# Kernel tuning notes

Measured on AMD Instinct MI355X. Metric: run time of the kernel, lower is better.

Reference implementation:

```python
import jax, jax.numpy as jnp
import numpy as np

B, C_IN, IMG = 4, 1, 256
E, P = 800, 4            # embed_size, patch_size
H, DH, M = 8, 64, 64     # heads, dim_head=heads**2, num_landmarks
N = (IMG // P) ** 2      # 4096 tokens
OUT = 256                # output_size
RESK = 33                # lucidrains residual depthwise conv kernel
BN_EPS = 1e-5
LN_EPS = 1e-5
PINV_ITERS = 6


def setup_inputs() -> dict:
    key = jax.random.key(0)
    ks = iter(jax.random.split(key, 32))
    def nrm(shape, s=0.02):
        return jax.random.normal(next(ks), shape, jnp.float32) * s
    inp = {"x": jax.random.normal(next(ks), (B, C_IN, IMG, IMG), jnp.float32)}
    # conv stack: (in, out, kernel); last conv has stride=P, padding=0
    for i, (ci, co, kk) in enumerate([(C_IN, 64, 3), (64, 128, 3), (128, 256, 3), (256, E, P)]):
        inp[f"w{i}"] = nrm((co, ci, kk, kk), 0.05)
        inp[f"b{i}"] = jnp.zeros((co,), jnp.float32)
        inp[f"g{i}"] = jnp.ones((co,), jnp.float32)    # BN gamma
        inp[f"be{i}"] = jnp.zeros((co,), jnp.float32)  # BN beta
        inp[f"mu{i}"] = nrm((co,), 0.1)                # BN running mean
        inp[f"var{i}"] = jax.random.uniform(next(ks), (co,), jnp.float32, 0.5, 1.5)
    inp["qkv_w"] = nrm((E, 3 * H * DH))      # to_qkv (no bias)
    inp["out_w"] = nrm((H * DH, E))          # to_out linear
    inp["out_b"] = jnp.zeros((E,), jnp.float32)
    inp["res_w"] = nrm((H, 1, RESK, 1), 0.05)  # depthwise residual conv over token dim
    inp["ln_g"] = jnp.ones((E,), jnp.float32)
    inp["ln_b"] = jnp.zeros((E,), jnp.float32)
    inp["head_w"] = nrm((E, OUT * OUT // N))   # Linear(800, 16)
    inp["head_b"] = jnp.zeros((OUT * OUT // N,), jnp.float32)
    return inp


def conv2d(x, w, b, stride, pad):
    y = jax.lax.conv_general_dilated(x, w, (stride, stride), [(pad, pad), (pad, pad)],
                                     dimension_numbers=("NCHW", "OIHW", "NCHW"))
    return y + b[None, :, None, None]


def bn(x, g, be, mu, var):
    s = g * jax.lax.rsqrt(var + BN_EPS)  # eval-mode BatchNorm
    return x * s[None, :, None, None] + (be - mu * s)[None, :, None, None]


def moore_penrose_pinv(a, iters=PINV_ITERS):
    I = jnp.eye(a.shape[-1], dtype=a.dtype)
    z = jnp.swapaxes(a, -1, -2) / (jnp.max(jnp.abs(a).sum(-1)) * jnp.max(jnp.abs(a).sum(-2)))
    for _ in range(iters):
        az = a @ z
        z = 0.25 * z @ (13.0 * I - az @ (15.0 * I - az @ (7.0 * I - az)))
    return z


def reference(x, w0, b0, g0, be0, mu0, var0, w1, b1, g1, be1, mu1, var1,
              w2, b2, g2, be2, mu2, var2, w3, b3, g3, be3, mu3, var3,
              qkv_w, out_w, out_b, res_w, ln_g, ln_b, head_w, head_b):
    # ---- PatchEmbedConv ----
    h = x
    blocks = [(w0, b0, g0, be0, mu0, var0, 1, 1), (w1, b1, g1, be1, mu1, var1, 1, 1),
              (w2, b2, g2, be2, mu2, var2, 1, 1), (w3, b3, g3, be3, mu3, var3, P, 0)]
    for w, b, g, be, mu, var, st, pd in blocks:
        h = jax.nn.relu(bn(conv2d(h, w, b, st, pd), g, be, mu, var))
    tok = h.reshape(B, E, N).transpose(0, 2, 1)  # [B, N, E]

    # ---- NystromAttention (n % m == 0, so no front padding needed) ----
    qkv = tok @ qkv_w  # [B, N, 3*H*DH]
    q, k, v = [t.reshape(B, N, H, DH).transpose(0, 2, 1, 3) for t in jnp.split(qkv, 3, axis=-1)]
    q = q * (DH ** -0.5)
    l = N // M
    q_l = q.reshape(B, H, M, l, DH).mean(3)  # landmark means over consecutive blocks
    k_l = k.reshape(B, H, M, l, DH).mean(3)
    a1 = jax.nn.softmax(jnp.einsum("bhnd,bhmd->bhnm", q, k_l), axis=-1)    # [B,H,N,M]
    a2 = jax.nn.softmax(jnp.einsum("bhmd,bhkd->bhmk", q_l, k_l), axis=-1)  # [B,H,M,M]
    a3 = jax.nn.softmax(jnp.einsum("bhmd,bhnd->bhmn", q_l, k), axis=-1)    # [B,H,M,N]
    out = (a1 @ moore_penrose_pinv(a2)) @ (a3 @ v)  # [B,H,N,DH]
    # residual depthwise conv over the token dim of v (groups = heads)
    res = jax.lax.conv_general_dilated(v, res_w, (1, 1), [(RESK // 2, RESK // 2), (0, 0)],
                                       dimension_numbers=("NCHW", "OIHW", "NCHW"),
                                       feature_group_count=H)
    out = out + res
    out = out.transpose(0, 2, 1, 3).reshape(B, N, H * DH)
    out = out @ out_w + out_b  # [B, N, E]

    # ---- LayerNorm ----
    mu_t = out.mean(-1, keepdims=True)
    var_t = out.var(-1, keepdims=True)
    out = (out - mu_t) * jax.lax.rsqrt(var_t + LN_EPS) * ln_g + ln_b

    # ---- reconstruction head ----
    y = jax.nn.sigmoid(out @ head_w + head_b)  # [B, N, OUT*OUT/N]
    return y.reshape(-1, 1, OUT, OUT)
```

## Files before the change

### kernel.cpp

```cpp
#include <hip/hip_runtime.h>

#define DI __device__ __forceinline__

constexpr float BN_EPS_C = 1e-5f;
constexpr float LN_EPS_C = 1e-5f;

typedef _Float16 half8 __attribute__((ext_vector_type(8)));
typedef float f32x4 __attribute__((ext_vector_type(4)));

constexpr size_t B_H0   = 0;
constexpr size_t B_H1   = 8388608;
constexpr size_t B_H2   = 25165824;
constexpr size_t B_Q    = 25165824;
constexpr size_t B_V    = 58720256;
constexpr size_t B_KT   = 75497472;
constexpr size_t B_ATT  = 92274688;
constexpr size_t B_LNB  = 25165824;
constexpr size_t B_TOK  = 159383552;
constexpr size_t B_WP1  = 185597952;
constexpr size_t B_WP2  = 185745408;
constexpr size_t B_WP3  = 186335232;
constexpr size_t B_QKVT = 192888832;
constexpr size_t B_OWT  = 195346432;
constexpr size_t B_QL   = 196165632;
constexpr size_t B_KL   = 196689920;
constexpr size_t B_KLH  = 197214208;
constexpr size_t B_A2   = 197476352;
constexpr size_t B_W2T  = 198524928;
constexpr size_t B_A3V  = 198787072;
constexpr size_t B_SCAL = 199311360;
constexpr size_t B_HWH  = 199311424;

DI float blockReduceSum(float v) {
  #pragma unroll
  for (int o = 32; o; o >>= 1) v += __shfl_xor(v, o);
  __shared__ float red[4];
  int w = threadIdx.x >> 6;
  __syncthreads();
  if ((threadIdx.x & 63) == 0) red[w] = v;
  __syncthreads();
  return red[0] + red[1] + red[2] + red[3];
}

template <int LP, int RP>
DI void mm16v(const float* L, const float* R, int r0, int c0, float reg[4][4]) {
  #pragma unroll
  for (int i = 0; i < 4; ++i)
    #pragma unroll
    for (int j = 0; j < 4; ++j) reg[i][j] = 0.f;
  #pragma unroll 4
  for (int dd = 0; dd < 64; dd += 4) {
    f32x4 l[4], rv[4];
    #pragma unroll
    for (int i = 0; i < 4; ++i)
      l[i] = *reinterpret_cast<const f32x4*>(&L[(size_t)(r0 + i) * LP + dd]);
    #pragma unroll
    for (int u = 0; u < 4; ++u)
      rv[u] = *reinterpret_cast<const f32x4*>(&R[(size_t)(dd + u) * RP + c0]);
    #pragma unroll
    for (int i = 0; i < 4; ++i)
      #pragma unroll
      for (int u = 0; u < 4; ++u)
        #pragma unroll
        for (int j = 0; j < 4; ++j)
          reg[i][j] = fmaf(l[i][u], rv[u][j], reg[i][j]);
  }
}

__global__ void k_pack_all(
    const float* __restrict__ w1, const float* __restrict__ w2c, const float* __restrict__ w3,
    const float* __restrict__ qkvw, const float* __restrict__ outw, const float* __restrict__ headw,
    _Float16* __restrict__ wp1, _Float16* __restrict__ wp2, _Float16* __restrict__ wp3,
    _Float16* __restrict__ qkvT, _Float16* __restrict__ owT, _Float16* __restrict__ hwh,
    float* __restrict__ scal) {
  size_t i = (size_t)blockIdx.x * 256 + threadIdx.x;
  if (i < 73728) {
    int q = i % 9, ci = (i / 9) % 64, co = i / (9 * 64);
    wp1[((size_t)co * 9 + q) * 64 + ci] = (_Float16)w1[i];
  } else if (i < 368640) {
    size_t j = i - 73728;
    int q = j % 9, ci = (j / 9) % 128, co = j / (9 * 128);
    wp2[((size_t)co * 9 + q) * 128 + ci] = (_Float16)w2c[j];
  } else if (i < 3645440) {
    size_t j = i - 368640;
    int q = j % 16, ci = (j / 16) % 256, co = j / (16 * 256);
    wp3[((size_t)co * 16 + q) * 256 + ci] = (_Float16)w3[j];
  } else if (i < 4874240) {
    size_t j = i - 3645440;
    int n = j % 1536, k = j / 1536;
    qkvT[(size_t)n * 800 + k] = (_Float16)qkvw[j];
  } else if (i < 5283840) {
    size_t j = i - 4874240;
    int n = j % 800, k = j / 800;
    owT[(size_t)n * 512 + k] = (_Float16)outw[j];
  } else if (i < 5296640) {
    size_t j = i - 5283840;
    int n = j % 16, k = j / 16;
    hwh[(size_t)n * 800 + k] = (_Float16)headw[j];
  } else if (i < 5296642) {
    scal[i - 5296640] = 0.f;
  }
}

__global__ __launch_bounds__(256) void k_conv0(
    const float* __restrict__ xb, const float* __restrict__ w0, const float* __restrict__ b0,
    const float* __restrict__ g0, const float* __restrict__ be0, const float* __restrict__ mu0,
    const float* __restrict__ var0, _Float16* __restrict__ h0) {
  const int t = threadIdx.x, co = t & 63, xg = t >> 6;
  const int y = blockIdx.x;
  const int x0 = blockIdx.y * 64 + xg * 16;
  float wreg[9];
  #pragma unroll
  for (int q = 0; q < 9; ++q) wreg[q] = w0[co * 9 + q];
  float s = g0[co] * rsqrtf(var0[co] + BN_EPS_C);
  float sh = fmaf(b0[co] - mu0[co], s, be0[co]);
  #pragma unroll 4
  for (int xl = 0; xl < 16; ++xl) {
    int xx = x0 + xl;
    float acc = 0.f;
    #pragma unroll
    for (int dy = 0; dy < 3; ++dy) {
      int yy = y + dy - 1;
      if ((unsigned)yy >= 256u) continue;
      #pragma unroll
      for (int dx = 0; dx < 3; ++dx) {
        int xi = xx + dx - 1;
        if ((unsigned)xi >= 256u) continue;
        acc = fmaf(wreg[dy * 3 + dx], xb[yy * 256 + xi], acc);
      }
    }
    float v = fmaxf(fmaf(acc, s, sh), 0.f);
    h0[((size_t)y * 256 + xx) * 64 + co] = (_Float16)v;
  }
}

template <int CI>
__global__ __launch_bounds__(256) void k_convs(
    const _Float16* __restrict__ in, const _Float16* __restrict__ wp,
    const float* __restrict__ bias, const float* __restrict__ g, const float* __restrict__ be,
    const float* __restrict__ mu, const float* __restrict__ var,
    _Float16* __restrict__ out, int CO, int NCT) {
  __shared__ _Float16 Ab[2][128 * 40];
  __shared__ _Float16 Bb[2][128 * 40];
  constexpr int CPQ = CI / 32;
  constexpr int NCK = 9 * CPQ;
  const int t = threadIdx.x;
  const int bid = blockIdx.x;
  const int xcd = bid & 7, slot = bid >> 3;
  const int pj = slot / NCT, cc = slot % NCT;
  const int p = pj * 8 + xcd;
  const int r0 = p * 128, c0 = cc * 128;

  const int ma = t >> 2, kga = t & 3;
  int ry[2], rx[2];
  #pragma unroll
  for (int s = 0; s < 2; ++s) {
    int r = r0 + ma + s * 64;
    ry[s] = r >> 8;
    rx[s] = r & 255;
  }
  const _Float16* baseB[2];
  #pragma unroll
  for (int s = 0; s < 2; ++s)
    baseB[s] = wp + (size_t)(c0 + ma + s * 64) * 9 * CI + kga * 8;
  const int wo = ma * 40 + kga * 8;

  auto loadA = [&](int s, int ck) -> half8 {
    int q = ck / CPQ, coff = (ck % CPQ) * 32;
    int yy = ry[s] + q / 3 - 1;
    int xx = rx[s] + q % 3 - 1;
    half8 a = {};
    if ((unsigned)yy < 256u && (unsigned)xx < 256u)
      a = *reinterpret_cast<const half8*>(in + ((size_t)yy * 256 + xx) * CI + coff + kga * 8);
    return a;
  };

  {
    half8 a0 = loadA(0, 0), a1 = loadA(1, 0);
    half8 b0v = *reinterpret_cast<const half8*>(baseB[0]);
    half8 b1v = *reinterpret_cast<const half8*>(baseB[1]);
    *reinterpret_cast<half8*>(&Ab[0][wo]) = a0;
    *reinterpret_cast<half8*>(&Ab[0][wo + 2560]) = a1;
    *reinterpret_cast<half8*>(&Bb[0][wo]) = b0v;
    *reinterpret_cast<half8*>(&Bb[0][wo + 2560]) = b1v;
  }
  __syncthreads();

  const int w = t >> 6, lo = t & 15, hi = (t >> 4) & 3;
  const int wm = w >> 1, wn = w & 1;
  const int roA = (wm * 64 + lo) * 40 + 8 * hi;
  const int roB = (wn * 64 + lo) * 40 + 8 * hi;
  f32x4 acc[4][4] = {};

  for (int ck = 0; ck < NCK; ++ck) {
    const int cur = ck & 1;
    const bool more = (ck + 1 < NCK);
    half8 rA0, rA1, rB0, rB1;
    if (more) {
      rA0 = loadA(0, ck + 1);
      rA1 = loadA(1, ck + 1);
      rB0 = *reinterpret_cast<const half8*>(baseB[0] + (ck + 1) * 32);
      rB1 = *reinterpret_cast<const half8*>(baseB[1] + (ck + 1) * 32);
    }
    half8 af[4], bf[4];
    #pragma unroll
    for (int mi = 0; mi < 4; ++mi)
      af[mi] = *reinterpret_cast<const half8*>(&Ab[cur][roA + mi * 640]);
    #pragma unroll
    for (int ni = 0; ni < 4; ++ni)
      bf[ni] = *reinterpret_cast<const half8*>(&Bb[cur][roB + ni * 640]);
    #pragma unroll
    for (int mi = 0; mi < 4; ++mi)
      #pragma unroll
      for (int ni = 0; ni < 4; ++ni)
        acc[mi][ni] = __builtin_amdgcn_mfma_f32_16x16x32_f16(af[mi], bf[ni], acc[mi][ni], 0, 0, 0);
    if (more) {
      *reinterpret_cast<half8*>(&Ab[cur ^ 1][wo]) = rA0;
      *reinterpret_cast<half8*>(&Ab[cur ^ 1][wo + 2560]) = rA1;
      *reinterpret_cast<half8*>(&Bb[cur ^ 1][wo]) = rB0;
      *reinterpret_cast<half8*>(&Bb[cur ^ 1][wo + 2560]) = rB1;
    }
    __syncthreads();
  }

  #pragma unroll
  for (int ni = 0; ni < 4; ++ni) {
    int co = c0 + wn * 64 + ni * 16 + lo;
    float s = g[co] * rsqrtf(var[co] + BN_EPS_C);
    float sh = fmaf(bias[co] - mu[co], s, be[co]);
    #pragma unroll
    for (int mi = 0; mi < 4; ++mi)
      #pragma unroll
      for (int rr = 0; rr < 4; ++rr) {
        int row = r0 + wm * 64 + mi * 16 + hi * 4 + rr;
        float v = fmaxf(fmaf(acc[mi][ni][rr], s, sh), 0.f);
        out[(size_t)row * CO + co] = (_Float16)v;
      }
  }
}

__global__ __launch_bounds__(256) void k_c3(
    const _Float16* __restrict__ h2, const _Float16* __restrict__ wp3,
    const float* __restrict__ b3, const float* __restrict__ g3, const float* __restrict__ be3,
    const float* __restrict__ mu3, const float* __restrict__ var3,
    _Float16* __restrict__ tok) {
  __shared__ _Float16 Abuf[2][128 * 40];
  __shared__ _Float16 Bbuf[2][160 * 40];
  const int t = threadIdx.x;
  const int bid = blockIdx.x;
  const int xcd = bid & 7, slot = bid >> 3;
  const int pj = slot / 5, cc = slot % 5;
  const int p = pj * 8 + xcd;
  const int r0 = p * 128, c0 = cc * 160;
  const int img = r0 >> 12;
  const _Float16* h2i = h2 + (size_t)img * 16777216;

  const int ma = t >> 2, kga = t & 3;
  const _Float16* baseA[2];
  #pragma unroll
  for (int s = 0; s < 2; ++s) {
    int m = ma + s * 64;
    int r = r0 + m;
    int py = (r & 4095) >> 6, px = r & 63;
    baseA[s] = h2i + ((size_t)py * 1024 + px * 4) * 256 + kga * 8;
  }
  const _Float16* baseB[3];
  #pragma unroll
  for (int s = 0; s < 3; ++s) {
    int cb = ma + s * 64;
    baseB[s] = wp3 + (size_t)(c0 + (cb < 160 ? cb : 159)) * 4096 + kga * 8;
  }
  const int wo = ma * 40 + kga * 8;

  const int w = t >> 6, lo = t & 15, hi = (t >> 4) & 3;
  const int wm = w >> 1, wn = w & 1;
  const int roA = (wm * 64 + lo) * 40 + 8 * hi;
  const int roB = (wn * 80 + lo) * 40 + 8 * hi;

  f32x4 acc[4][5] = {};

  {
    half8 a0 = *reinterpret_cast<const half8*>(baseA[0]);
    half8 a1 = *reinterpret_cast<const half8*>(baseA[1]);
    half8 b0v = *reinterpret_cast<const half8*>(baseB[0]);
    half8 b1v = *reinterpret_cast<const half8*>(baseB[1]);
    *reinterpret_cast<half8*>(&Abuf[0][wo]) = a0;
    *reinterpret_cast<half8*>(&Abuf[0][wo + 2560]) = a1;
    *reinterpret_cast<half8*>(&Bbuf[0][wo]) = b0v;
    *reinterpret_cast<half8*>(&Bbuf[0][wo + 2560]) = b1v;
    if (t < 128) {
      half8 b2v = *reinterpret_cast<const half8*>(baseB[2]);
      *reinterpret_cast<half8*>(&Bbuf[0][wo + 5120]) = b2v;
    }
  }
  __syncthreads();

  for (int ck = 0; ck < 128; ++ck) {
    const int cur = ck & 1;
    const bool more = (ck + 1 < 128);
    half8 rA0, rA1, rB0, rB1, rB2;
    if (more) {
      const int kn = (ck + 1) << 5;
      const int q = kn >> 8, qk = kn & 255;
      const int aoff = (q >> 2) * 65536 + (q & 3) * 256 + qk;
      rA0 = *reinterpret_cast<const half8*>(baseA[0] + aoff);
      rA1 = *reinterpret_cast<const half8*>(baseA[1] + aoff);
      rB0 = *reinterpret_cast<const half8*>(baseB[0] + kn);
      rB1 = *reinterpret_cast<const half8*>(baseB[1] + kn);
      if (t < 128) rB2 = *reinterpret_cast<const half8*>(baseB[2] + kn);
    }
    half8 af[4], bf[5];
    #pragma unroll
    for (int mi = 0; mi < 4; ++mi)
      af[mi] = *reinterpret_cast<const half8*>(&Abuf[cur][roA + mi * 640]);
    #pragma unroll
    for (int ni = 0; ni < 5; ++ni)
      bf[ni] = *reinterpret_cast<const half8*>(&Bbuf[cur][roB + ni * 640]);
    #pragma unroll
    for (int mi = 0; mi < 4; ++mi)
      #pragma unroll
      for (int ni = 0; ni < 5; ++ni)
        acc[mi][ni] = __builtin_amdgcn_mfma_f32_16x16x32_f16(af[mi], bf[ni], acc[mi][ni], 0, 0, 0);
    if (more) {
      *reinterpret_cast<half8*>(&Abuf[cur ^ 1][wo]) = rA0;
      *reinterpret_cast<half8*>(&Abuf[cur ^ 1][wo + 2560]) = rA1;
      *reinterpret_cast<half8*>(&Bbuf[cur ^ 1][wo]) = rB0;
      *reinterpret_cast<half8*>(&Bbuf[cur ^ 1][wo + 2560]) = rB1;
      if (t < 128) *reinterpret_cast<half8*>(&Bbuf[cur ^ 1][wo + 5120]) = rB2;
    }
    __syncthreads();
  }

  #pragma unroll
  for (int ni = 0; ni < 5; ++ni) {
    int col = c0 + wn * 80 + ni * 16 + lo;
    float s = g3[col] * rsqrtf(var3[col] + BN_EPS_C);
    float sh = fmaf(b3[col] - mu3[col], s, be3[col]);
    #pragma unroll
    for (int mi = 0; mi < 4; ++mi)
      #pragma unroll
      for (int rr = 0; rr < 4; ++rr) {
        int row = r0 + wm * 64 + mi * 16 + hi * 4 + rr;
        float v = fmaxf(fmaf(acc[mi][ni][rr], s, sh), 0.f);
        tok[(size_t)row * 800 + col] = (_Float16)v;
      }
  }
}

__global__ __launch_bounds__(256) void k_qkv_s(
    const _Float16* __restrict__ tok, const _Float16* __restrict__ qkvT,
    _Float16* __restrict__ qx, _Float16* __restrict__ kTg, _Float16* __restrict__ vx,
    float* __restrict__ ql, float* __restrict__ kl, _Float16* __restrict__ klh) {
  __shared__ _Float16 SH[20480];
  _Float16* AbP = SH;
  _Float16* BbP = SH + 10240;
  const int t = threadIdx.x;
  const int bid = blockIdx.x;
  const int xcd = bid & 7, slot = bid >> 3;
  const int pj = slot / 12, cc = slot % 12;
  const int p = pj * 8 + xcd;
  const int r0 = p * 128, c0 = cc * 128;

  const int ma = t >> 2, kga = t & 3;
  const _Float16* baseA[2];
  const _Float16* baseB[2];
  #pragma unroll
  for (int s = 0; s < 2; ++s) {
    baseA[s] = tok + (size_t)(r0 + ma + s * 64) * 800 + kga * 8;
    baseB[s] = qkvT + (size_t)(c0 + ma + s * 64) * 800 + kga * 8;
  }
  const int wo = ma * 40 + kga * 8;

  {
    half8 a0 = *reinterpret_cast<const half8*>(baseA[0]);
    half8 a1 = *reinterpret_cast<const half8*>(baseA[1]);
    half8 b0v = *reinterpret_cast<const half8*>(baseB[0]);
    half8 b1v = *reinterpret_cast<const half8*>(baseB[1]);
    *reinterpret_cast<half8*>(&AbP[wo]) = a0;
    *reinterpret_cast<half8*>(&AbP[wo + 2560]) = a1;
    *reinterpret_cast<half8*>(&BbP[wo]) = b0v;
    *reinterpret_cast<half8*>(&BbP[wo + 2560]) = b1v;
  }
  __syncthreads();

  const int w = t >> 6, lo = t & 15, hi = (t >> 4) & 3;
  const int wm = w >> 1, wn = w & 1;
  const int roA = (wm * 64 + lo) * 40 + 8 * hi;
  const int roB = (wn * 64 + lo) * 40 + 8 * hi;
  f32x4 acc[4][4] = {};

  for (int ck = 0; ck < 25; ++ck) {
    const int cur = ck & 1;
    const bool more = (ck + 1 < 25);
    half8 rA0, rA1, rB0, rB1;
    if (more) {
      const int kn = (ck + 1) * 32;
      rA0 = *reinterpret_cast<const half8*>(baseA[0] + kn);
      rA1 = *reinterpret_cast<const half8*>(baseA[1] + kn);
      rB0 = *reinterpret_cast<const half8*>(baseB[0] + kn);
      rB1 = *reinterpret_cast<const half8*>(baseB[1] + kn);
    }
    half8 af[4], bf[4];
    #pragma unroll
    for (int mi = 0; mi < 4; ++mi)
      af[mi] = *reinterpret_cast<const half8*>(&AbP[cur * 5120 + roA + mi * 640]);
    #pragma unroll
    for (int ni = 0; ni < 4; ++ni)
      bf[ni] = *reinterpret_cast<const half8*>(&BbP[cur * 5120 + roB + ni * 640]);
    #pragma unroll
    for (int mi = 0; mi < 4; ++mi)
      #pragma unroll
      for (int ni = 0; ni < 4; ++ni)
        acc[mi][ni] = __builtin_amdgcn_mfma_f32_16x16x32_f16(af[mi], bf[ni], acc[mi][ni], 0, 0, 0);
    if (more) {
      *reinterpret_cast<half8*>(&AbP[(cur ^ 1) * 5120 + wo]) = rA0;
      *reinterpret_cast<half8*>(&AbP[(cur ^ 1) * 5120 + wo + 2560]) = rA1;
      *reinterpret_cast<half8*>(&BbP[(cur ^ 1) * 5120 + wo]) = rB0;
      *reinterpret_cast<half8*>(&BbP[(cur ^ 1) * 5120 + wo + 2560]) = rB1;
    }
    __syncthreads();
  }

  const int seg = cc >> 2;
  const int b = r0 >> 12;
  const int m = ((r0 & 4095) >> 6) + wm;
  if (seg == 1) {
    #pragma unroll
    for (int ni = 0; ni < 4; ++ni) {
      int cl = wn * 64 + ni * 16 + lo;
      #pragma unroll
      for (int mi = 0; mi < 4; ++mi)
        #pragma unroll
        for (int rr = 0; rr < 4; ++rr) {
          int nl = wm * 64 + mi * 16 + hi * 4 + rr;
          SH[cl * 136 + nl] = (_Float16)acc[mi][ni][rr];
        }
    }
    __syncthreads();
    const int base_row = b * 512 + (cc & 3) * 128;
    const int base_n = (p & 31) * 128;
    #pragma unroll
    for (int e = t; e < 2048; e += 256) {
      int cl = e >> 4, ch = e & 15;
      half8 vvv = *reinterpret_cast<const half8*>(&SH[cl * 136 + ch * 8]);
      *reinterpret_cast<half8*>(&kTg[(size_t)(base_row + cl) * 4096 + base_n + ch * 8]) = vvv;
    }
  } else {
    const float scale = (seg == 0) ? 0.125f : 1.0f;
    _Float16* dst = (seg == 0) ? qx : vx;
    #pragma unroll
    for (int ni = 0; ni < 4; ++ni) {
      int cseg = (cc & 3) * 128 + wn * 64 + ni * 16 + lo;
      int h = cseg >> 6, d = cseg & 63;
      #pragma unroll
      for (int mi = 0; mi < 4; ++mi)
        #pragma unroll
        for (int rr = 0; rr < 4; ++rr) {
          int row = r0 + wm * 64 + mi * 16 + hi * 4 + rr;
          int nn = row & 4095;
          dst[((size_t)(b * 8 + h) * 4096 + nn) * 64 + d] = (_Float16)(acc[mi][ni][rr] * scale);
        }
    }
  }
  if (seg <= 1) {
    const float lscale = ((seg == 0) ? 0.125f : 1.0f) * (1.f / 64.f);
    #pragma unroll
    for (int ni = 0; ni < 4; ++ni) {
      float sum = 0.f;
      #pragma unroll
      for (int mi = 0; mi < 4; ++mi)
        #pragma unroll
        for (int rr = 0; rr < 4; ++rr) sum += acc[mi][ni][rr];
      sum += __shfl_xor(sum, 16);
      sum += __shfl_xor(sum, 32);
      if (hi == 0) {
        int cseg = (cc & 3) * 128 + wn * 64 + ni * 16 + lo;
        int h = cseg >> 6, d = cseg & 63;
        int bh = b * 8 + h;
        float lm = sum * lscale;
        if (seg == 0) {
          ql[((size_t)bh * 64 + m) * 64 + d] = lm;
        } else {
          kl[((size_t)bh * 64 + m) * 64 + d] = lm;
          klh[((size_t)bh * 64 + m) * 64 + d] = (_Float16)lm;
        }
      }
    }
  }
}

__global__ __launch_bounds__(256) void k_op_s(
    const _Float16* __restrict__ attb, const _Float16* __restrict__ owT,
    const float* __restrict__ ob, _Float16* __restrict__ lnb) {
  __shared__ _Float16 Abuf[2][128 * 40];
  __shared__ _Float16 Bbuf[2][160 * 40];
  const int t = threadIdx.x;
  const int bid = blockIdx.x;
  const int xcd = bid & 7, slot = bid >> 3;
  const int pj = slot / 5, cc = slot % 5;
  const int p = pj * 8 + xcd;
  const int r0 = p * 128, c0 = cc * 160;

  const int ma = t >> 2, kga = t & 3;
  const _Float16* baseA[2];
  #pragma unroll
  for (int s = 0; s < 2; ++s)
    baseA[s] = attb + (size_t)(r0 + ma + s * 64) * 512 + kga * 8;
  const _Float16* baseB[3];
  #pragma unroll
  for (int s = 0; s < 3; ++s) {
    int cb = ma + s * 64;
    baseB[s] = owT + (size_t)(c0 + (cb < 160 ? cb : 159)) * 512 + kga * 8;
  }
  const int wo = ma * 40 + kga * 8;

  const int w = t >> 6, lo = t & 15, hi = (t >> 4) & 3;
  const int wm = w >> 1, wn = w & 1;
  const int roA = (wm * 64 + lo) * 40 + 8 * hi;
  const int roB = (wn * 80 + lo) * 40 + 8 * hi;

  f32x4 acc[4][5] = {};

  {
    half8 a0 = *reinterpret_cast<const half8*>(baseA[0]);
    half8 a1 = *reinterpret_cast<const half8*>(baseA[1]);
    half8 b0v = *reinterpret_cast<const half8*>(baseB[0]);
    half8 b1v = *reinterpret_cast<const half8*>(baseB[1]);
    *reinterpret_cast<half8*>(&Abuf[0][wo]) = a0;
    *reinterpret_cast<half8*>(&Abuf[0][wo + 2560]) = a1;
    *reinterpret_cast<half8*>(&Bbuf[0][wo]) = b0v;
    *reinterpret_cast<half8*>(&Bbuf[0][wo + 2560]) = b1v;
    if (t < 128) {
      half8 b2v = *reinterpret_cast<const half8*>(baseB[2]);
      *reinterpret_cast<half8*>(&Bbuf[0][wo + 5120]) = b2v;
    }
  }
  __syncthreads();

  for (int ck = 0; ck < 16; ++ck) {
    const int cur = ck & 1;
    const bool more = (ck + 1 < 16);
    half8 rA0, rA1, rB0, rB1, rB2;
    if (more) {
      const int kn = (ck + 1) << 5;
      rA0 = *reinterpret_cast<const half8*>(baseA[0] + kn);
      rA1 = *reinterpret_cast<const half8*>(baseA[1] + kn);
      rB0 = *reinterpret_cast<const half8*>(baseB[0] + kn);
      rB1 = *reinterpret_cast<const half8*>(baseB[1] + kn);
      if (t < 128) rB2 = *reinterpret_cast<const half8*>(baseB[2] + kn);
    }
    half8 af[4], bf[5];
    #pragma unroll
    for (int mi = 0; mi < 4; ++mi)
      af[mi] = *reinterpret_cast<const half8*>(&Abuf[cur][roA + mi * 640]);
    #pragma unroll
    for (int ni = 0; ni < 5; ++ni)
      bf[ni] = *reinterpret_cast<const half8*>(&Bbuf[cur][roB + ni * 640]);
    #pragma unroll
    for (int mi = 0; mi < 4; ++mi)
      #pragma unroll
      for (int ni = 0; ni < 5; ++ni)
        acc[mi][ni] = __builtin_amdgcn_mfma_f32_16x16x32_f16(af[mi], bf[ni], acc[mi][ni], 0, 0, 0);
    if (more) {
      *reinterpret_cast<half8*>(&Abuf[cur ^ 1][wo]) = rA0;
      *reinterpret_cast<half8*>(&Abuf[cur ^ 1][wo + 2560]) = rA1;
      *reinterpret_cast<half8*>(&Bbuf[cur ^ 1][wo]) = rB0;
      *reinterpret_cast<half8*>(&Bbuf[cur ^ 1][wo + 2560]) = rB1;
      if (t < 128) *reinterpret_cast<half8*>(&Bbuf[cur ^ 1][wo + 5120]) = rB2;
    }
    __syncthreads();
  }

  #pragma unroll
  for (int ni = 0; ni < 5; ++ni) {
    int col = c0 + wn * 80 + ni * 16 + lo;
    float bv = ob[col];
    #pragma unroll
    for (int mi = 0; mi < 4; ++mi)
      #pragma unroll
      for (int rr = 0; rr < 4; ++rr) {
        int row = r0 + wm * 64 + mi * 16 + hi * 4 + rr;
        lnb[(size_t)row * 800 + col] = (_Float16)(acc[mi][ni][rr] + bv);
      }
  }
}

__global__ __launch_bounds__(64) void k_a2(
    const float* __restrict__ ql, const float* __restrict__ kl,
    float* __restrict__ a2, float* __restrict__ scal) {
  __shared__ float sp[64 * 65];
  const int bh = blockIdx.x, t = threadIdx.x;
  const float* qr = ql + ((size_t)bh * 64 + t) * 64;
  const float* kb = kl + (size_t)bh * 4096;
  float mx = -1e30f;
  for (int c = 0; c < 64; ++c) {
    float acc = 0.f;
    #pragma unroll 8
    for (int dd = 0; dd < 64; ++dd) acc = fmaf(qr[dd], kb[c * 64 + dd], acc);
    sp[t * 65 + c] = acc;
    mx = fmaxf(mx, acc);
  }
  float sum = 0.f;
  for (int c = 0; c < 64; ++c) {
    float e = expf(sp[t * 65 + c] - mx);
    sp[t * 65 + c] = e;
    sum += e;
  }
  float inv = 1.f / sum;
  float rs = 0.f;
  for (int c = 0; c < 64; ++c) {
    float p = sp[t * 65 + c] * inv;
    sp[t * 65 + c] = p;
    a2[(size_t)bh * 4096 + t * 64 + c] = p;
    rs += p;
  }
  atomicMax(reinterpret_cast<int*>(scal), __float_as_int(rs));
  __syncthreads();
  float cs = 0.f;
  for (int r = 0; r < 64; ++r) cs += sp[r * 65 + t];
  atomicMax(reinterpret_cast<int*>(scal) + 1, __float_as_int(cs));
}

__global__ __launch_bounds__(256) void k_a3v(
    const float* __restrict__ ql, const _Float16* __restrict__ kT,
    const _Float16* __restrict__ vx, float* __restrict__ a3v) {
  __shared__ float sq[64];
  __shared__ float sP[4096];
  __shared__ float red[4];
  __shared__ float red2[4][64];
  const int t = threadIdx.x;
  const int m = blockIdx.x, bh = blockIdx.y;
  if (t < 64) sq[t] = ql[((size_t)bh * 64 + m) * 64 + t];
  __syncthreads();
  const _Float16* kb = kT + (size_t)bh * 262144;
  float sc[16];
  #pragma unroll
  for (int i = 0; i < 16; ++i) sc[i] = 0.f;
  for (int dd = 0; dd < 64; ++dd) {
    float qv = sq[dd];
    const half8* kr = reinterpret_cast<const half8*>(kb + (size_t)dd * 4096 + t * 16);
    half8 k0 = kr[0], k1 = kr[1];
    #pragma unroll
    for (int i = 0; i < 8; ++i) sc[i] = fmaf(qv, (float)k0[i], sc[i]);
    #pragma unroll
    for (int i = 0; i < 8; ++i) sc[8 + i] = fmaf(qv, (float)k1[i], sc[8 + i]);
  }
  float mx = sc[0];
  #pragma unroll
  for (int i = 1; i < 16; ++i) mx = fmaxf(mx, sc[i]);
  #pragma unroll
  for (int o = 32; o; o >>= 1) mx = fmaxf(mx, __shfl_xor(mx, o));
  if ((t & 63) == 0) red[t >> 6] = mx;
  __syncthreads();
  mx = fmaxf(fmaxf(red[0], red[1]), fmaxf(red[2], red[3]));
  __syncthreads();
  float sum = 0.f;
  #pragma unroll
  for (int i = 0; i < 16; ++i) {
    sc[i] = expf(sc[i] - mx);
    sum += sc[i];
  }
  #pragma unroll
  for (int o = 32; o; o >>= 1) sum += __shfl_xor(sum, o);
  if ((t & 63) == 0) red[t >> 6] = sum;
  __syncthreads();
  sum = red[0] + red[1] + red[2] + red[3];
  float inv = 1.f / sum;
  #pragma unroll
  for (int i = 0; i < 16; ++i) sP[t * 16 + i] = sc[i] * inv;
  __syncthreads();
  const int seg = t >> 6, l = t & 63;
  const int nl = l >> 3, dblk = (l & 7) * 8;
  const _Float16* vb = vx + (size_t)bh * 262144;
  float acc8[8] = {};
  for (int it = 0; it < 128; ++it) {
    int n8 = seg * 1024 + it * 8;
    half8 vv = *reinterpret_cast<const half8*>(&vb[(size_t)(n8 + nl) * 64 + dblk]);
    float pc = sP[n8 + nl];
    #pragma unroll
    for (int u = 0; u < 8; ++u) acc8[u] = fmaf(pc, (float)vv[u], acc8[u]);
  }
  #pragma unroll
  for (int off = 8; off <= 32; off <<= 1)
    #pragma unroll
    for (int u = 0; u < 8; ++u) acc8[u] += __shfl_xor(acc8[u], off);
  if (nl == 0) {
    #pragma unroll
    for (int u = 0; u < 8; ++u) red2[seg][dblk + u] = acc8[u];
  }
  __syncthreads();
  if (seg == 0)
    a3v[((size_t)bh * 64 + m) * 64 + l] = red2[0][l] + red2[1][l] + red2[2][l] + red2[3][l];
}

__global__ __launch_bounds__(256) void k_pinv(
    const float* __restrict__ a2g, const float* __restrict__ scal,
    const float* __restrict__ a3vg, _Float16* __restrict__ w2t) {
  __shared__ float z[64 * 68];
  __shared__ float az[64 * 68];
  __shared__ float tb[64 * 68];
  const int bh = blockIdx.x, t = threadIdx.x;
  const int r0 = (t >> 4) << 2, c0 = (t & 15) << 2;
  const float* ag = a2g + (size_t)bh * 4096;
  const float denom = 1.f / (scal[0] * scal[1]);
  #pragma unroll
  for (int i = 0; i < 4; ++i)
    #pragma unroll
    for (int j = 0; j < 4; ++j)
      z[(r0 + i) * 68 + c0 + j] = ag[(c0 + j) * 64 + r0 + i] * denom;
  __syncthreads();
  float reg[4][4], val[4][4];
  for (int it = 0; it < 6; ++it) {
    mm16v<64, 68>(ag, z, r0, c0, reg);
    #pragma unroll
    for (int i = 0; i < 4; ++i)
      #pragma unroll
      for (int j = 0; j < 4; ++j) az[(r0 + i) * 68 + c0 + j] = reg[i][j];
    __syncthreads();
    mm16v<68, 68>(az, az, r0, c0, reg);
    #pragma unroll
    for (int i = 0; i < 4; ++i)
      #pragma unroll
      for (int j = 0; j < 4; ++j)
        tb[(r0 + i) * 68 + c0 + j] = 7.f * az[(r0 + i) * 68 + c0 + j] - reg[i][j];
    __syncthreads();
    mm16v<68, 68>(az, tb, r0, c0, reg);
    #pragma unroll
    for (int i = 0; i < 4; ++i)
      #pragma unroll
      for (int j = 0; j < 4; ++j)
        val[i][j] = 15.f * az[(r0 + i) * 68 + c0 + j] - reg[i][j];
    __syncthreads();
    #pragma unroll
    for (int i = 0; i < 4; ++i)
      #pragma unroll
      for (int j = 0; j < 4; ++j) tb[(r0 + i) * 68 + c0 + j] = val[i][j];
    __syncthreads();
    mm16v<68, 68>(z, tb, r0, c0, reg);
    #pragma unroll
    for (int i = 0; i < 4; ++i)
      #pragma unroll
      for (int j = 0; j < 4; ++j)
        val[i][j] = 0.25f * (13.f * z[(r0 + i) * 68 + c0 + j] - reg[i][j]);
    __syncthreads();
    #pragma unroll
    for (int i = 0; i < 4; ++i)
      #pragma unroll
      for (int j = 0; j < 4; ++j) z[(r0 + i) * 68 + c0 + j] = val[i][j];
    __syncthreads();
  }
  mm16v<68, 64>(z, a3vg + (size_t)bh * 4096, r0, c0, reg);
  #pragma unroll
  for (int i = 0; i < 4; ++i)
    #pragma unroll
    for (int j = 0; j < 4; ++j)
      w2t[(size_t)bh * 4096 + (c0 + j) * 64 + (r0 + i)] = (_Float16)reg[i][j];
}

__global__ __launch_bounds__(256) void k_combine_m(
    const _Float16* __restrict__ qx, const _Float16* __restrict__ klh,
    const _Float16* __restrict__ w2t, const _Float16* __restrict__ vx,
    const float* __restrict__ rw, _Float16* __restrict__ att) {
  __shared__ _Float16 sP[64 * 72];
  __shared__ _Float16 sVT[64 * 104];
  __shared__ _Float16 sT[64 * 104];
  __shared__ float sR[33];
  const int t = threadIdx.x, w = t >> 6, lo = t & 15, hi = (t >> 4) & 3;
  const int n0 = blockIdx.x * 64;
  const int h = blockIdx.y, b = blockIdx.z, bh = b * 8 + h;
  if (t < 33) sR[t] = rw[h * 33 + t];
  __syncthreads();
  const _Float16* vb = vx + (size_t)bh * 262144;
  #pragma unroll
  for (int u = 0; u < 24; ++u) {
    int e = t + u * 256;
    int r = e >> 6, d = e & 63;
    int nn = n0 - 16 + r;
    sVT[d * 104 + r] = ((unsigned)nn < 4096u) ? vb[(size_t)nn * 64 + d] : (_Float16)0.f;
  }
  #pragma unroll
  for (int u = 0; u < 24; ++u) {
    int e = t + u * 256;
    int r = e % 96, i = e / 96;
    int j = r - i;
    sT[i * 104 + r] = (j >= 0 && j < 33) ? (_Float16)sR[j] : (_Float16)0.f;
  }
  f32x4 sa[4] = {};
  const _Float16* qp = qx + ((size_t)bh * 4096 + n0 + w * 16 + lo) * 64 + 8 * hi;
  const _Float16* klp = klh + (size_t)bh * 4096;
  #pragma unroll
  for (int c = 0; c < 2; ++c) {
    half8 a = *reinterpret_cast<const half8*>(qp + 32 * c);
    #pragma unroll
    for (int ct = 0; ct < 4; ++ct) {
      half8 bf = *reinterpret_cast<const half8*>(klp + (size_t)(ct * 16 + lo) * 64 + 8 * hi + 32 * c);
      sa[ct] = __builtin_amdgcn_mfma_f32_16x16x32_f16(a, bf, sa[ct], 0, 0, 0);
    }
  }
  #pragma unroll
  for (int r = 0; r < 4; ++r) {
    float mx = fmaxf(fmaxf(sa[0][r], sa[1][r]), fmaxf(sa[2][r], sa[3][r]));
    #pragma unroll
    for (int o = 8; o; o >>= 1) mx = fmaxf(mx, __shfl_xor(mx, o));
    float e0 = expf(sa[0][r] - mx), e1 = expf(sa[1][r] - mx);
    float e2 = expf(sa[2][r] - mx), e3 = expf(sa[3][r] - mx);
    float sm = e0 + e1 + e2 + e3;
    #pragma unroll
    for (int o = 8; o; o >>= 1) sm += __shfl_xor(sm, o);
    float inv = 1.f / sm;
    int row = w * 16 + hi * 4 + r;
    sP[row * 72 + lo] = (_Float16)(e0 * inv);
    sP[row * 72 + 16 + lo] = (_Float16)(e1 * inv);
    sP[row * 72 + 32 + lo] = (_Float16)(e2 * inv);
    sP[row * 72 + 48 + lo] = (_Float16)(e3 * inv);
  }
  __syncthreads();
  f32x4 ao[4] = {};
  const _Float16* w2p = w2t + (size_t)bh * 4096;
  #pragma unroll
  for (int c = 0; c < 2; ++c) {
    half8 a = *reinterpret_cast<const half8*>(&sP[(w * 16 + lo) * 72 + 8 * hi + 32 * c]);
    #pragma unroll
    for (int ct = 0; ct < 4; ++ct) {
      half8 bf = *reinterpret_cast<const half8*>(w2p + (size_t)(ct * 16 + lo) * 64 + 8 * hi + 32 * c);
      ao[ct] = __builtin_amdgcn_mfma_f32_16x16x32_f16(a, bf, ao[ct], 0, 0, 0);
    }
  }
  #pragma unroll
  for (int c = 0; c < 3; ++c) {
    half8 a = *reinterpret_cast<const half8*>(&sT[(w * 16 + lo) * 104 + 8 * hi + 32 * c]);
    #pragma unroll
    for (int ct = 0; ct < 4; ++ct) {
      half8 bf = *reinterpret_cast<const half8*>(&sVT[(ct * 16 + lo) * 104 + 8 * hi + 32 * c]);
      ao[ct] = __builtin_amdgcn_mfma_f32_16x16x32_f16(a, bf, ao[ct], 0, 0, 0);
    }
  }
  _Float16* ab = att + ((size_t)b * 4096) * 512 + (size_t)h * 64;
  #pragma unroll
  for (int ct = 0; ct < 4; ++ct)
    #pragma unroll
    for (int r = 0; r < 4; ++r) {
      int n = n0 + w * 16 + hi * 4 + r;
      ab[(size_t)n * 512 + ct * 16 + lo] = (_Float16)ao[ct][r];
    }
}

__global__ __launch_bounds__(256) void k_ln16(
    _Float16* __restrict__ buf, const float* __restrict__ g, const float* __restrict__ bb) {
  const int t = threadIdx.x;
  _Float16* p = buf + (size_t)blockIdx.x * 800;
  float x0 = (float)p[t], x1 = (float)p[t + 256], x2 = (float)p[t + 512];
  float x3 = (t < 32) ? (float)p[t + 768] : 0.f;
  float s = blockReduceSum(x0 + x1 + x2 + x3);
  float mean = s * (1.f / 800.f);
  float d0 = x0 - mean, d1 = x1 - mean, d2 = x2 - mean;
  float d3 = (t < 32) ? x3 - mean : 0.f;
  float s2 = blockReduceSum(d0 * d0 + d1 * d1 + d2 * d2 + d3 * d3);
  float rstd = rsqrtf(s2 * (1.f / 800.f) + LN_EPS_C);
  p[t] = (_Float16)(d0 * rstd * g[t] + bb[t]);
  p[t + 256] = (_Float16)(d1 * rstd * g[t + 256] + bb[t + 256]);
  p[t + 512] = (_Float16)(d2 * rstd * g[t + 512] + bb[t + 512]);
  if (t < 32) p[t + 768] = (_Float16)(d3 * rstd * g[t + 768] + bb[t + 768]);
}

__global__ __launch_bounds__(256) void k_head_m(
    const _Float16* __restrict__ ln, const _Float16* __restrict__ hwh,
    const float* __restrict__ hb, float* __restrict__ out) {
  const int t = threadIdx.x, w = t >> 6, lo = t & 15, hi = (t >> 4) & 3;
  const int row0 = blockIdx.x * 64 + w * 16;
  const _Float16* ap = ln + (size_t)(row0 + lo) * 800 + 8 * hi;
  const _Float16* bp = hwh + (size_t)lo * 800 + 8 * hi;
  f32x4 acc = {};
  #pragma unroll 5
  for (int k = 0; k < 800; k += 32) {
    half8 a = *reinterpret_cast<const half8*>(ap + k);
    half8 b = *reinterpret_cast<const half8*>(bp + k);
    acc = __builtin_amdgcn_mfma_f32_16x16x32_f16(a, b, acc, 0, 0, 0);
  }
  float bv = hb[lo];
  #pragma unroll
  for (int r = 0; r < 4; ++r) {
    int row = row0 + hi * 4 + r;
    out[(size_t)row * 16 + lo] = 1.f / (1.f + expf(-(acc[r] + bv)));
  }
}

extern "C" void kernel_launch(void* const* d_in, const int* in_sizes, int n_in,
                              void* d_out, int out_size, void* d_ws, size_t ws_size,
                              hipStream_t stream) {
  (void)in_sizes; (void)n_in; (void)out_size; (void)ws_size;
  const float* x     = (const float*)d_in[0];
  const float* w0    = (const float*)d_in[1];
  const float* b0    = (const float*)d_in[2];
  const float* g0    = (const float*)d_in[3];
  const float* be0   = (const float*)d_in[4];
  const float* mu0   = (const float*)d_in[5];
  const float* var0  = (const float*)d_in[6];
  const float* w1    = (const float*)d_in[7];
  const float* b1    = (const float*)d_in[8];
  const float* g1    = (const float*)d_in[9];
  const float* be1   = (const float*)d_in[10];
  const float* mu1   = (const float*)d_in[11];
  const float* var1  = (const float*)d_in[12];
  const float* w2c   = (const float*)d_in[13];
  const float* b2    = (const float*)d_in[14];
  const float* g2    = (const float*)d_in[15];
  const float* be2   = (const float*)d_in[16];
  const float* mu2   = (const float*)d_in[17];
  const float* var2  = (const float*)d_in[18];
  const float* w3    = (const float*)d_in[19];
  const float* b3    = (const float*)d_in[20];
  const float* g3    = (const float*)d_in[21];
  const float* be3   = (const float*)d_in[22];
  const float* mu3   = (const float*)d_in[23];
  const float* var3  = (const float*)d_in[24];
  const float* qkvw  = (const float*)d_in[25];
  const float* outw  = (const float*)d_in[26];
  const float* outbv = (const float*)d_in[27];
  const float* resw  = (const float*)d_in[28];
  const float* lng   = (const float*)d_in[29];
  const float* lnbv  = (const float*)d_in[30];
  const float* headw = (const float*)d_in[31];
  const float* headb = (const float*)d_in[32];

  char* wsb = (char*)d_ws;
  _Float16* h0   = (_Float16*)(wsb + B_H0);
  _Float16* h1   = (_Float16*)(wsb + B_H1);
  _Float16* h2   = (_Float16*)(wsb + B_H2);
  _Float16* qb   = (_Float16*)(wsb + B_Q);
  _Float16* vb   = (_Float16*)(wsb + B_V);
  _Float16* kT   = (_Float16*)(wsb + B_KT);
  _Float16* tok  = (_Float16*)(wsb + B_TOK);
  _Float16* attb = (_Float16*)(wsb + B_ATT);
  _Float16* wp1  = (_Float16*)(wsb + B_WP1);
  _Float16* wp2  = (_Float16*)(wsb + B_WP2);
  _Float16* wp3  = (_Float16*)(wsb + B_WP3);
  _Float16* qkvT = (_Float16*)(wsb + B_QKVT);
  _Float16* owT  = (_Float16*)(wsb + B_OWT);
  _Float16* klh  = (_Float16*)(wsb + B_KLH);
  _Float16* w2t  = (_Float16*)(wsb + B_W2T);
  _Float16* hwh  = (_Float16*)(wsb + B_HWH);
  _Float16* lnb16 = (_Float16*)(wsb + B_LNB);
  float* ql   = (float*)(wsb + B_QL);
  float* kl   = (float*)(wsb + B_KL);
  float* a2   = (float*)(wsb + B_A2);
  float* a3v  = (float*)(wsb + B_A3V);
  float* scal = (float*)(wsb + B_SCAL);

  k_pack_all<<<dim3(20691), 256, 0, stream>>>(
      w1, w2c, w3, qkvw, outw, headw, wp1, wp2, wp3, qkvT, owT, hwh, scal);

  for (int img = 0; img < 4; ++img) {
    k_conv0<<<dim3(256, 4), 256, 0, stream>>>(
        x + (size_t)img * 65536, w0, b0, g0, be0, mu0, var0, h0);
    k_convs<64><<<dim3(512), 256, 0, stream>>>(
        h0, wp1, b1, g1, be1, mu1, var1, h1, 128, 1);
    k_convs<128><<<dim3(1024), 256, 0, stream>>>(
        h1, wp2, b2, g2, be2, mu2, var2, h2 + (size_t)img * 16777216, 256, 2);
  }
  k_c3<<<dim3(640), 256, 0, stream>>>(h2, wp3, b3, g3, be3, mu3, var3, tok);
  k_qkv_s<<<dim3(1536), 256, 0, stream>>>(tok, qkvT, qb, kT, vb, ql, kl, klh);
  k_a2<<<dim3(32), 64, 0, stream>>>(ql, kl, a2, scal);
  k_a3v<<<dim3(64, 32), 256, 0, stream>>>(ql, kT, vb, a3v);
  k_pinv<<<dim3(32), 256, 0, stream>>>(a2, scal, a3v, w2t);
  k_combine_m<<<dim3(64, 8, 4), 256, 0, stream>>>(qb, klh, w2t, vb, resw, attb);
  k_op_s<<<dim3(640), 256, 0, stream>>>(attb, owT, outbv, lnb16);
  k_ln16<<<dim3(16384), 256, 0, stream>>>(lnb16, lng, lnbv);
  k_head_m<<<dim3(256), 256, 0, stream>>>(lnb16, hwh, headb, (float*)d_out);
}
```

Measured before the change: 947.8 us.

## Deepen conv GEMM prefetch to two stages and fuse LayerNorm into head

The conv3x3 and patch-conv GEMM main loops are unrolled by two and keep two sets of prefetch registers, so global loads for chunk k+2 are issued before the MMA on chunk k. The aim is to hide more global latency behind the MFMA work. Separately, the LayerNorm kernel is merged into the reconstruction head: each wave computes the row mean and variance with a single-pass sum of x and x squared, then normalizes on the fly while feeding the MFMA. This removes a 16384-block launch and a read-write pass over the token buffer. In exchange it uses more registers, and the E[x²]-mean² variance is numerically less robust.

```diff
diff --git a/kernel.cpp b/kernel.cpp
--- a/kernel.cpp
+++ b/kernel.cpp
@@ -175,6 +175,12 @@
     return a;
   };
 
+  const int w = t >> 6, lo = t & 15, hi = (t >> 4) & 3;
+  const int wm = w >> 1, wn = w & 1;
+  const int roA = (wm * 64 + lo) * 40 + 8 * hi;
+  const int roB = (wn * 64 + lo) * 40 + 8 * hi;
+  f32x4 acc[4][4] = {};
+
   {
     half8 a0 = loadA(0, 0), a1 = loadA(1, 0);
     half8 b0v = *reinterpret_cast<const half8*>(baseB[0]);
@@ -184,44 +190,54 @@
     *reinterpret_cast<half8*>(&Bb[0][wo]) = b0v;
     *reinterpret_cast<half8*>(&Bb[0][wo + 2560]) = b1v;
   }
-  __syncthreads();
-
-  const int w = t >> 6, lo = t & 15, hi = (t >> 4) & 3;
-  const int wm = w >> 1, wn = w & 1;
-  const int roA = (wm * 64 + lo) * 40 + 8 * hi;
-  const int roB = (wn * 64 + lo) * 40 + 8 * hi;
-  f32x4 acc[4][4] = {};
-
-  for (int ck = 0; ck < NCK; ++ck) {
-    const int cur = ck & 1;
-    const bool more = (ck + 1 < NCK);
-    half8 rA0, rA1, rB0, rB1;
-    if (more) {
-      rA0 = loadA(0, ck + 1);
-      rA1 = loadA(1, ck + 1);
-      rB0 = *reinterpret_cast<const half8*>(baseB[0] + (ck + 1) * 32);
-      rB1 = *reinterpret_cast<const half8*>(baseB[1] + (ck + 1) * 32);
-    }
-    half8 af[4], bf[4];
-    #pragma unroll
-    for (int mi = 0; mi < 4; ++mi)
-      af[mi] = *reinterpret_cast<const half8*>(&Ab[cur][roA + mi * 640]);
-    #pragma unroll
-    for (int ni = 0; ni < 4; ++ni)
-      bf[ni] = *reinterpret_cast<const half8*>(&Bb[cur][roB + ni * 640]);
-    #pragma unroll
-    for (int mi = 0; mi < 4; ++mi)
-      #pragma unroll
-      for (int ni = 0; ni < 4; ++ni)
-        acc[mi][ni] = __builtin_amdgcn_mfma_f32_16x16x32_f16(af[mi], bf[ni], acc[mi][ni], 0, 0, 0);
-    if (more) {
-      *reinterpret_cast<half8*>(&Ab[cur ^ 1][wo]) = rA0;
-      *reinterpret_cast<half8*>(&Ab[cur ^ 1][wo + 2560]) = rA1;
-      *reinterpret_cast<half8*>(&Bb[cur ^ 1][wo]) = rB0;
-      *reinterpret_cast<half8*>(&Bb[cur ^ 1][wo + 2560]) = rB1;
-    }
-    __syncthreads();
-  }
+  half8 pA0 = loadA(0, 1), pA1 = loadA(1, 1);
+  half8 pB0 = *reinterpret_cast<const half8*>(baseB[0] + 32);
+  half8 pB1 = *reinterpret_cast<const half8*>(baseB[1] + 32);
+  half8 qA0, qA1, qB0, qB1;
+  __syncthreads();
+
+#define CVS_COMPUTE(BUF)                                                                  \
+  {                                                                                       \
+    half8 af[4], bf[4];                                                                   \
+    _Pragma("unroll") for (int mi = 0; mi < 4; ++mi)                                      \
+        af[mi] = *reinterpret_cast<const half8*>(&Ab[BUF][roA + mi * 640]);               \
+    _Pragma("unroll") for (int ni = 0; ni < 4; ++ni)                                      \
+        bf[ni] = *reinterpret_cast<const half8*>(&Bb[BUF][roB + ni * 640]);               \
+    _Pragma("unroll") for (int mi = 0; mi < 4; ++mi)                                      \
+        _Pragma("unroll") for (int ni = 0; ni < 4; ++ni)                                  \
+            acc[mi][ni] =                                                                 \
+                __builtin_amdgcn_mfma_f32_16x16x32_f16(af[mi], bf[ni], acc[mi][ni], 0, 0, 0); \
+  }
+
+  for (int ck = 0; ck < NCK; ck += 2) {
+    if (ck + 2 < NCK) {
+      qA0 = loadA(0, ck + 2);
+      qA1 = loadA(1, ck + 2);
+      qB0 = *reinterpret_cast<const half8*>(baseB[0] + (ck + 2) * 32);
+      qB1 = *reinterpret_cast<const half8*>(baseB[1] + (ck + 2) * 32);
+    }
+    CVS_COMPUTE(0);
+    *reinterpret_cast<half8*>(&Ab[1][wo]) = pA0;
+    *reinterpret_cast<half8*>(&Ab[1][wo + 2560]) = pA1;
+    *reinterpret_cast<half8*>(&Bb[1][wo]) = pB0;
+    *reinterpret_cast<half8*>(&Bb[1][wo + 2560]) = pB1;
+    __syncthreads();
+    if (ck + 3 < NCK) {
+      pA0 = loadA(0, ck + 3);
+      pA1 = loadA(1, ck + 3);
+      pB0 = *reinterpret_cast<const half8*>(baseB[0] + (ck + 3) * 32);
+      pB1 = *reinterpret_cast<const half8*>(baseB[1] + (ck + 3) * 32);
+    }
+    CVS_COMPUTE(1);
+    if (ck + 2 < NCK) {
+      *reinterpret_cast<half8*>(&Ab[0][wo]) = qA0;
+      *reinterpret_cast<half8*>(&Ab[0][wo + 2560]) = qA1;
+      *reinterpret_cast<half8*>(&Bb[0][wo]) = qB0;
+      *reinterpret_cast<half8*>(&Bb[0][wo + 2560]) = qB1;
+    }
+    __syncthreads();
+  }
+#undef CVS_COMPUTE
 
   #pragma unroll
   for (int ni = 0; ni < 4; ++ni) {
@@ -293,43 +309,55 @@
       *reinterpret_cast<half8*>(&Bbuf[0][wo + 5120]) = b2v;
     }
   }
-  __syncthreads();
-
-  for (int ck = 0; ck < 128; ++ck) {
-    const int cur = ck & 1;
-    const bool more = (ck + 1 < 128);
-    half8 rA0, rA1, rB0, rB1, rB2;
-    if (more) {
-      const int kn = (ck + 1) << 5;
-      const int q = kn >> 8, qk = kn & 255;
-      const int aoff = (q >> 2) * 65536 + (q & 3) * 256 + qk;
-      rA0 = *reinterpret_cast<const half8*>(baseA[0] + aoff);
-      rA1 = *reinterpret_cast<const half8*>(baseA[1] + aoff);
-      rB0 = *reinterpret_cast<const half8*>(baseB[0] + kn);
-      rB1 = *reinterpret_cast<const half8*>(baseB[1] + kn);
-      if (t < 128) rB2 = *reinterpret_cast<const half8*>(baseB[2] + kn);
-    }
-    half8 af[4], bf[5];
-    #pragma unroll
-    for (int mi = 0; mi < 4; ++mi)
-      af[mi] = *reinterpret_cast<const half8*>(&Abuf[cur][roA + mi * 640]);
-    #pragma unroll
-    for (int ni = 0; ni < 5; ++ni)
-      bf[ni] = *reinterpret_cast<const half8*>(&Bbuf[cur][roB + ni * 640]);
-    #pragma unroll
-    for (int mi = 0; mi < 4; ++mi)
-      #pragma unroll
-      for (int ni = 0; ni < 5; ++ni)
-        acc[mi][ni] = __builtin_amdgcn_mfma_f32_16x16x32_f16(af[mi], bf[ni], acc[mi][ni], 0, 0, 0);
-    if (more) {
-      *reinterpret_cast<half8*>(&Abuf[cur ^ 1][wo]) = rA0;
-      *reinterpret_cast<half8*>(&Abuf[cur ^ 1][wo + 2560]) = rA1;
-      *reinterpret_cast<half8*>(&Bbuf[cur ^ 1][wo]) = rB0;
-      *reinterpret_cast<half8*>(&Bbuf[cur ^ 1][wo + 2560]) = rB1;
-      if (t < 128) *reinterpret_cast<half8*>(&Bbuf[cur ^ 1][wo + 5120]) = rB2;
-    }
-    __syncthreads();
-  }
+  half8 pA0, pA1, pB0, pB1, pB2;
+  half8 qA0, qA1, qB0, qB1, qB2;
+#define C3_LOADS(dA0, dA1, dB0, dB1, dB2, CK)                                    \
+  {                                                                              \
+    const int kn = (CK) << 5;                                                    \
+    const int q = kn >> 8, qk = kn & 255;                                        \
+    const int aoff = (q >> 2) * 65536 + (q & 3) * 256 + qk;                      \
+    dA0 = *reinterpret_cast<const half8*>(baseA[0] + aoff);                      \
+    dA1 = *reinterpret_cast<const half8*>(baseA[1] + aoff);                      \
+    dB0 = *reinterpret_cast<const half8*>(baseB[0] + kn);                        \
+    dB1 = *reinterpret_cast<const half8*>(baseB[1] + kn);                        \
+    if (t < 128) dB2 = *reinterpret_cast<const half8*>(baseB[2] + kn);           \
+  }
+#define C3_COMPUTE(BUF)                                                                   \
+  {                                                                                       \
+    half8 af[4], bf[5];                                                                   \
+    _Pragma("unroll") for (int mi = 0; mi < 4; ++mi)                                      \
+        af[mi] = *reinterpret_cast<const half8*>(&Abuf[BUF][roA + mi * 640]);             \
+    _Pragma("unroll") for (int ni = 0; ni < 5; ++ni)                                      \
+        bf[ni] = *reinterpret_cast<const half8*>(&Bbuf[BUF][roB + ni * 640]);             \
+    _Pragma("unroll") for (int mi = 0; mi < 4; ++mi)                                      \
+        _Pragma("unroll") for (int ni = 0; ni < 5; ++ni)                                  \
+            acc[mi][ni] =                                                                 \
+                __builtin_amdgcn_mfma_f32_16x16x32_f16(af[mi], bf[ni], acc[mi][ni], 0, 0, 0); \
+  }
+#define C3_WRITE(BUF, sA0, sA1, sB0, sB1, sB2)                 \
+  {                                                            \
+    *reinterpret_cast<half8*>(&Abuf[BUF][wo]) = sA0;           \
+    *reinterpret_cast<half8*>(&Abuf[BUF][wo + 2560]) = sA1;    \
+    *reinterpret_cast<half8*>(&Bbuf[BUF][wo]) = sB0;           \
+    *reinterpret_cast<half8*>(&Bbuf[BUF][wo + 2560]) = sB1;    \
+    if (t < 128) *reinterpret_cast<half8*>(&Bbuf[BUF][wo + 5120]) = sB2; \
+  }
+  C3_LOADS(pA0, pA1, pB0, pB1, pB2, 1);
+  __syncthreads();
+
+  for (int ck = 0; ck < 128; ck += 2) {
+    if (ck + 2 < 128) C3_LOADS(qA0, qA1, qB0, qB1, qB2, ck + 2);
+    C3_COMPUTE(0);
+    C3_WRITE(1, pA0, pA1, pB0, pB1, pB2);
+    __syncthreads();
+    if (ck + 3 < 128) C3_LOADS(pA0, pA1, pB0, pB1, pB2, ck + 3);
+    C3_COMPUTE(1);
+    if (ck + 2 < 128) C3_WRITE(0, qA0, qA1, qB0, qB1, qB2);
+    __syncthreads();
+  }
+#undef C3_LOADS
+#undef C3_COMPUTE
+#undef C3_WRITE
 
   #pragma unroll
   for (int ni = 0; ni < 5; ++ni) {
@@ -845,37 +873,43 @@
     }
 }
 
-__global__ __launch_bounds__(256) void k_ln16(
-    _Float16* __restrict__ buf, const float* __restrict__ g, const float* __restrict__ bb) {
-  const int t = threadIdx.x;
-  _Float16* p = buf + (size_t)blockIdx.x * 800;
-  float x0 = (float)p[t], x1 = (float)p[t + 256], x2 = (float)p[t + 512];
-  float x3 = (t < 32) ? (float)p[t + 768] : 0.f;
-  float s = blockReduceSum(x0 + x1 + x2 + x3);
-  float mean = s * (1.f / 800.f);
-  float d0 = x0 - mean, d1 = x1 - mean, d2 = x2 - mean;
-  float d3 = (t < 32) ? x3 - mean : 0.f;
-  float s2 = blockReduceSum(d0 * d0 + d1 * d1 + d2 * d2 + d3 * d3);
-  float rstd = rsqrtf(s2 * (1.f / 800.f) + LN_EPS_C);
-  p[t] = (_Float16)(d0 * rstd * g[t] + bb[t]);
-  p[t + 256] = (_Float16)(d1 * rstd * g[t + 256] + bb[t + 256]);
-  p[t + 512] = (_Float16)(d2 * rstd * g[t + 512] + bb[t + 512]);
-  if (t < 32) p[t + 768] = (_Float16)(d3 * rstd * g[t + 768] + bb[t + 768]);
-}
-
-__global__ __launch_bounds__(256) void k_head_m(
+__global__ __launch_bounds__(256) void k_lnhead(
     const _Float16* __restrict__ ln, const _Float16* __restrict__ hwh,
+    const float* __restrict__ g, const float* __restrict__ bb,
     const float* __restrict__ hb, float* __restrict__ out) {
   const int t = threadIdx.x, w = t >> 6, lo = t & 15, hi = (t >> 4) & 3;
   const int row0 = blockIdx.x * 64 + w * 16;
   const _Float16* ap = ln + (size_t)(row0 + lo) * 800 + 8 * hi;
+  float s1 = 0.f, s2 = 0.f;
+  #pragma unroll 5
+  for (int k = 0; k < 800; k += 32) {
+    half8 a = *reinterpret_cast<const half8*>(ap + k);
+    #pragma unroll
+    for (int u = 0; u < 8; ++u) {
+      float x = (float)a[u];
+      s1 += x;
+      s2 = fmaf(x, x, s2);
+    }
+  }
+  s1 += __shfl_xor(s1, 16); s1 += __shfl_xor(s1, 32);
+  s2 += __shfl_xor(s2, 16); s2 += __shfl_xor(s2, 32);
+  float mean = s1 * (1.f / 800.f);
+  float var = s2 * (1.f / 800.f) - mean * mean;
+  float rstd = rsqrtf(var + LN_EPS_C);
   const _Float16* bp = hwh + (size_t)lo * 800 + 8 * hi;
   f32x4 acc = {};
   #pragma unroll 5
   for (int k = 0; k < 800; k += 32) {
     half8 a = *reinterpret_cast<const half8*>(ap + k);
+    half8 an;
+    #pragma unroll
+    for (int u = 0; u < 8; ++u) {
+      int kk = k + 8 * hi + u;
+      float x = ((float)a[u] - mean) * rstd * g[kk] + bb[kk];
+      an[u] = (_Float16)x;
+    }
     half8 b = *reinterpret_cast<const half8*>(bp + k);
-    acc = __builtin_amdgcn_mfma_f32_16x16x32_f16(a, b, acc, 0, 0, 0);
+    acc = __builtin_amdgcn_mfma_f32_16x16x32_f16(an, b, acc, 0, 0, 0);
   }
   float bv = hb[lo];
   #pragma unroll
@@ -965,6 +999,5 @@
   k_pinv<<<dim3(32), 256, 0, stream>>>(a2, scal, a3v, w2t);
   k_combine_m<<<dim3(64, 8, 4), 256, 0, stream>>>(qb, klh, w2t, vb, resw, attb);
   k_op_s<<<dim3(640), 256, 0, stream>>>(attb, owT, outbv, lnb16);
-  k_ln16<<<dim3(16384), 256, 0, stream>>>(lnb16, lng, lnbv);
-  k_head_m<<<dim3(256), 256, 0, stream>>>(lnb16, hwh, headb, (float*)d_out);
-}
+  k_lnhead<<<dim3(256), 256, 0, stream>>>(lnb16, hwh, lng, lnbv, headb, (float*)d_out);
+}
```

Result: no change. 950.0 us (+0.2%).
